# Kernel tuning notes

Measured on AMD Instinct MI355X. Metric: run time of the kernel, lower is better.

The kernel has to match this reference:

```python
import jax, jax.numpy as jnp
import numpy as np

B, N, C, NH = 32, 1024, 768, 12
KS = 3
KK = KS * KS
HD = C // NH
SCALE = HD ** -0.5
PMD = 2 * C   # patch_mix_dims = int(2 * dim)
CMD = 2 * C   # channel_mix_dims = int(2 * dim)


def _ln(x, g, b, eps):
    m = jnp.mean(x, axis=-1, keepdims=True)
    v = jnp.var(x, axis=-1, keepdims=True)
    return (x - m) * jax.lax.rsqrt(v + eps) * g + b


def setup_inputs() -> dict:
    key = jax.random.key(0)
    ks = jax.random.split(key, 12)
    w = lambda k, shape: jax.random.normal(k, shape, jnp.float32) * 0.02
    return dict(
        x=jax.random.normal(ks[0], (B, N, C), jnp.float32),
        H=32, W=32,
        kernel=w(ks[1], (KK, C)),                 # nn.Parameter, std 0.02
        ln_g=jnp.ones((C,), jnp.float32), ln_b=jnp.zeros((C,), jnp.float32),
        kv_w=w(ks[2], (C, 2 * C)),                # kv Linear, no bias (qkv_bias=False)
        proj_w=w(ks[3], (C, C)), proj_b=jnp.zeros((C,), jnp.float32),
        projq_w=w(ks[4], (C, C)),                 # proj_q, no bias
        n1_g=jnp.ones((C,), jnp.float32), n1_b=jnp.zeros((C,), jnp.float32),
        n2_g=jnp.ones((C,), jnp.float32), n2_b=jnp.zeros((C,), jnp.float32),
        pm1_w=w(ks[5], (KK, PMD)), pm1_b=jnp.zeros((PMD,), jnp.float32),
        pm2_w=w(ks[6], (PMD, KK)), pm2_b=jnp.zeros((KK,), jnp.float32),
        cm1_w=w(ks[7], (C, CMD)), cm1_b=jnp.zeros((CMD,), jnp.float32),
        cm2_w=w(ks[8], (CMD, C)), cm2_b=jnp.zeros((C,), jnp.float32),
    )


def reference(x, H, W, kernel, ln_g, ln_b, kv_w, proj_w, proj_b, projq_w,
              n1_g, n1_b, n2_g, n2_b, pm1_w, pm1_b, pm2_w, pm2_b,
              cm1_w, cm1_b, cm2_w, cm2_b):
    Bv, Nv, Cv = x.shape
    # w: expand learned 3x3 token kernel to batch -> [B, 9, C]
    w0 = jnp.broadcast_to(kernel, (Bv, KK, Cv))
    # queries from LN(kernel): [B, nh, 9, hd]
    wm = _ln(w0, ln_g, ln_b, 1e-6).reshape(Bv, KK, NH, HD).transpose(0, 2, 1, 3)
    # keys/values from x: [B, nh, N, hd]
    kv = (x @ kv_w).reshape(Bv, Nv, 2, NH, HD)
    k = kv[:, :, 0].transpose(0, 2, 1, 3)
    v = kv[:, :, 1].transpose(0, 2, 1, 3)
    attn = jax.nn.softmax(jnp.einsum('bhqd,bhkd->bhqk', wm, k) * SCALE, axis=-1)
    ca = jnp.einsum('bhqk,bhkd->bhqd', attn, v).transpose(0, 2, 1, 3).reshape(Bv, KK, Cv)
    ca = ca @ proj_w + proj_b
    w1 = w0 + ca                                  # [B, 9, C]
    # MLPMixer layer (drop_path = 0 -> identity)
    t = _ln(w1, n1_g, n1_b, 1e-5).transpose(0, 2, 1)              # [B, C, 9]
    t = jax.nn.gelu(t @ pm1_w + pm1_b, approximate=False) @ pm2_w + pm2_b
    w1 = w1 + t.transpose(0, 2, 1)
    t = _ln(w1, n2_g, n2_b, 1e-5)
    w1 = w1 + (jax.nn.gelu(t @ cm1_w + cm1_b, approximate=False) @ cm2_w + cm2_b)
    # dynamic per-(batch,channel) 3x3 depthwise conv
    filt = w1.transpose(0, 2, 1).reshape(Bv * Cv, 1, KS, KS)       # [B*C, 1, 3, 3]
    xq = (x @ projq_w).transpose(0, 2, 1).reshape(1, Bv * Cv, H, W)
    y = jax.lax.conv_general_dilated(
        xq, filt, window_strides=(1, 1), padding=((1, 1), (1, 1)),
        feature_group_count=Bv * Cv,
        dimension_numbers=('NCHW', 'OIHW', 'NCHW'))
    return y.reshape(Bv, Cv, H * W).transpose(0, 2, 1)             # [B, N, C]
```

## Files before the change

### kernel.cpp

```cpp
#include <hip/hip_runtime.h>
#include <hip/hip_bf16.h>
#include <cstdint>
#include <cstddef>

typedef __attribute__((ext_vector_type(8))) short bf16x8;
typedef __attribute__((ext_vector_type(4))) float f32x4;

#define BB 32
#define NN 1024
#define CC 768
#define NHH 12
#define HDD 64
#define KKK 9
#define MM (BB * NN)
#define KN2 1664
#define PMDD 1536
#define CMDD 1536
#define BK 64

#define XBF_BLOCKS 12288
#define WT_BLOCKS 1152
#define WT2_BLOCKS 2880
#define SW_BLOCKS 128

__device__ __forceinline__ float bfbits2f(short s) {
  union { uint32_t u; float f; } cv;
  cv.u = ((uint32_t)(uint16_t)s) << 16;
  return cv.f;
}
__device__ __forceinline__ short f2bf(float f) {
  union { float f; uint32_t u; } cv;
  cv.f = f;
  uint32_t u = cv.u;
  uint32_t r = (u + 0x7fffu + ((u >> 16) & 1u)) >> 16;
  return (short)r;
}
__device__ __forceinline__ float gelu_f(float x) {
  return 0.5f * x * (1.0f + erff(x * 0.7071067811865476f));
}

typedef const __attribute__((address_space(1))) uint32_t* gp1_t;
typedef __attribute__((address_space(3))) uint32_t* lp3_t;
__device__ __forceinline__ void gload16(const short* g, const short* l) {
  __builtin_amdgcn_global_load_lds((gp1_t)(uintptr_t)(const void*)g,
                                   (lp3_t)(uint32_t)(uintptr_t)(const void*)l,
                                   16, 0, 0);
}

__global__ __launch_bounds__(256) void prep_kernel(
    const float* __restrict__ x, short* __restrict__ xb,
    const float* __restrict__ kv_w, const float* __restrict__ projq_w,
    short* __restrict__ Wt,
    const float* __restrict__ proj_w, const float* __restrict__ cm1_w,
    const float* __restrict__ cm2_w,
    short* __restrict__ WpT, short* __restrict__ Wc1T, short* __restrict__ Wc2T,
    const float* __restrict__ kern, const float* __restrict__ ln_g,
    const float* __restrict__ ln_b)
{
  __shared__ float smem[1056];
  const int bx = blockIdx.x;
  const int tid = threadIdx.x;
  if (bx < XBF_BLOCKS) {
    const int i = (bx * 256 + tid) * 8;
    f32x4 a = *(const f32x4*)&x[i];
    f32x4 b = *(const f32x4*)&x[i + 4];
    bf16x8 o;
#pragma unroll
    for (int e = 0; e < 4; e++) { o[e] = f2bf(a[e]); o[e + 4] = f2bf(b[e]); }
    *(bf16x8*)&xb[i] = o;
    return;
  }
  if (bx < XBF_BLOCKS + WT_BLOCKS) {
    int b2 = bx - XBF_BLOCKS;
    int j0 = (b2 % 48) * 32;
    int c0 = (b2 / 48) * 32;
    const float* src; int ldj, jj;
    if (j0 < 768) { src = kv_w; ldj = 1536; jj = 768 + j0; }
    else          { src = projq_w; ldj = 768; jj = j0 - 768; }
    const int tx = tid & 31, ty = tid >> 5;
#pragma unroll
    for (int r = 0; r < 4; r++) {
      int cl = ty + r * 8;
      smem[cl * 33 + tx] = src[(size_t)(c0 + cl) * ldj + jj + tx];
    }
    __syncthreads();
#pragma unroll
    for (int r = 0; r < 4; r++) {
      int jl = ty + r * 8;
      Wt[(size_t)(j0 + jl) * CC + c0 + tx] = f2bf(smem[tx * 33 + jl]);
    }
    return;
  }
  if (bx < XBF_BLOCKS + WT_BLOCKS + WT2_BLOCKS) {
    int b2 = bx - XBF_BLOCKS - WT_BLOCKS;
    const float* src; short* dst; int ldj, ldc, j0, c0;
    if (b2 < 576)        { src = proj_w; dst = WpT;  ldj = 768;  ldc = 768;
                           j0 = (b2 % 24) * 32; c0 = (b2 / 24) * 32; }
    else if (b2 < 1728)  { b2 -= 576; src = cm1_w; dst = Wc1T; ldj = 1536; ldc = 768;
                           j0 = (b2 % 48) * 32; c0 = (b2 / 48) * 32; }
    else                 { b2 -= 1728; src = cm2_w; dst = Wc2T; ldj = 768; ldc = 1536;
                           j0 = (b2 % 24) * 32; c0 = (b2 / 24) * 32; }
    const int tx = tid & 31, ty = tid >> 5;
#pragma unroll
    for (int r = 0; r < 4; r++) {
      int cl = ty + r * 8;
      smem[cl * 33 + tx] = src[(size_t)(c0 + cl) * ldj + j0 + tx];
    }
    __syncthreads();
#pragma unroll
    for (int r = 0; r < 4; r++) {
      int jl = ty + r * 8;
      dst[(size_t)(j0 + jl) * ldc + c0 + tx] = f2bf(smem[tx * 33 + jl]);
    }
    return;
  }
  {
    const int s = bx - (XBF_BLOCKS + WT_BLOCKS + WT2_BLOCKS);
    if (s >= 108) {
      const size_t r = (size_t)(1536 + s) * CC;
      Wt[r + tid] = 0; Wt[r + tid + 256] = 0; Wt[r + tid + 512] = 0;
      return;
    }
    const int h = s / 9, q = s % 9;
    float* red = smem;
    const size_t base = (size_t)q * CC;
    float x0 = kern[base + tid];
    float x1 = kern[base + tid + 256];
    float x2 = kern[base + tid + 512];
    red[tid] = x0 + x1 + x2;
    __syncthreads();
    for (int st = 128; st > 0; st >>= 1) { if (tid < st) red[tid] += red[tid + st]; __syncthreads(); }
    float mean = red[0] * (1.0f / 768.0f);
    __syncthreads();
    float d0 = x0 - mean, d1 = x1 - mean, d2 = x2 - mean;
    red[tid] = d0 * d0 + d1 * d1 + d2 * d2;
    __syncthreads();
    for (int st = 128; st > 0; st >>= 1) { if (tid < st) red[tid] += red[tid + st]; __syncthreads(); }
    float rstd = rsqrtf(red[0] * (1.0f / 768.0f) + 1e-6f);
    __syncthreads();
    smem[tid]       = d0 * rstd * ln_g[tid]       + ln_b[tid];
    smem[tid + 256] = d1 * rstd * ln_g[tid + 256] + ln_b[tid + 256];
    smem[tid + 512] = d2 * rstd * ln_g[tid + 512] + ln_b[tid + 512];
    __syncthreads();
#pragma unroll
    for (int k = 0; k < 3; k++) {
      const int cc = tid + k * 256;
      const float* kw = &kv_w[(size_t)cc * 1536 + h * HDD];
      float acc = 0.f;
#pragma unroll
      for (int dd = 0; dd < HDD; dd++) acc += smem[h * HDD + dd] * kw[dd];
      Wt[(size_t)(1536 + s) * CC + cc] = f2bf(acc * 0.125f);
    }
  }
}

__global__ __launch_bounds__(256) void gemm_bt_kernel(
    const short* __restrict__ A,
    const short* __restrict__ Bt,
    short* __restrict__ C)
{
  __shared__ short As[128 * BK];
  __shared__ short Bs[128 * BK];
  const int tid = threadIdx.x;
  const int wave = tid >> 6, lane = tid & 63;
  const int lid = blockIdx.x;
  const int wid = (lid & 7) * 416 + (lid >> 3);
  const int bn = (wid % 13) * 128;
  const int bm = (wid / 13) * 128;
  const int wmo = (wave >> 1) * 64;
  const int wno = (wave & 1) * 64;
  const int lrow = lane & 15;
  const int kgrp = lane >> 4;
  const int sr = tid >> 3;
  const int ss = tid & 7;
  const int slotG = ss ^ (sr & 7);
  const short* gA = A + (size_t)(bm + sr) * CC + slotG * 8;
  const short* gB = Bt + (size_t)(bn + sr) * CC + slotG * 8;
  const short* lA = &As[sr * BK + ss * 8];
  const short* lB = &Bs[sr * BK + ss * 8];
  const int rs0 = kgrp ^ (lrow & 7);
  const int rs1 = (4 + kgrp) ^ (lrow & 7);
  f32x4 acc[4][4];
#pragma unroll
  for (int i = 0; i < 4; i++)
#pragma unroll
    for (int j = 0; j < 4; j++) acc[i][j] = (f32x4){0.f, 0.f, 0.f, 0.f};
  for (int k0 = 0; k0 < CC; k0 += BK) {
    __syncthreads();
#pragma unroll
    for (int i = 0; i < 4; i++) {
      gload16(gA + (size_t)(i * 32) * CC + k0, lA + i * 32 * BK);
      gload16(gB + (size_t)(i * 32) * CC + k0, lB + i * 32 * BK);
    }
    __syncthreads();
#pragma unroll
    for (int kh = 0; kh < 2; kh++) {
      const int rs = kh ? rs1 : rs0;
      bf16x8 af[4], bfr[4];
#pragma unroll
      for (int i = 0; i < 4; i++)
        af[i] = *(const bf16x8*)&As[(wmo + i * 16 + lrow) * BK + rs * 8];
#pragma unroll
      for (int j = 0; j < 4; j++)
        bfr[j] = *(const bf16x8*)&Bs[(wno + j * 16 + lrow) * BK + rs * 8];
#pragma unroll
      for (int i = 0; i < 4; i++)
#pragma unroll
        for (int j = 0; j < 4; j++)
          acc[i][j] = __builtin_amdgcn_mfma_f32_16x16x32_bf16(af[i], bfr[j], acc[i][j], 0, 0, 0);
    }
  }
#pragma unroll
  for (int i = 0; i < 4; i++)
#pragma unroll
    for (int j = 0; j < 4; j++)
#pragma unroll
      for (int r = 0; r < 4; r++) {
        const int row = bm + wmo + i * 16 + kgrp * 4 + r;
        const int col = bn + wno + j * 16 + lrow;
        C[(size_t)row * KN2 + col] = f2bf(acc[i][j][r]);
      }
}

template <int EP>
__global__ __launch_bounds__(256) void mfma96_kernel(
    const short* __restrict__ A,
    const short* __restrict__ Bt,
    int K, int ldn,
    const float* __restrict__ bias,
    const float* __restrict__ kern,
    float* __restrict__ Cf,
    short* __restrict__ Cb)
{
  __shared__ short As[96 * BK];
  __shared__ short Bs[128 * BK];
  const int tid = threadIdx.x;
  const int wave = tid >> 6, lane = tid & 63;
  const int bm = blockIdx.x * 96;
  const int bn = blockIdx.y * 128;
  const int wmo = (wave >> 1) * 48;
  const int wno = (wave & 1) * 64;
  const int lrow = lane & 15;
  const int kgrp = lane >> 4;
  const int sr = tid >> 3;
  const int ss = tid & 7;
  const int rs0 = kgrp ^ (lrow & 7);
  const int rs1 = (4 + kgrp) ^ (lrow & 7);
  f32x4 acc[3][4];
#pragma unroll
  for (int i = 0; i < 3; i++)
#pragma unroll
    for (int j = 0; j < 4; j++) acc[i][j] = (f32x4){0.f, 0.f, 0.f, 0.f};
  for (int k0 = 0; k0 < K; k0 += BK) {
    __syncthreads();
#pragma unroll
    for (int i = 0; i < 3; i++) {
      const int r = i * 32 + sr;
      const int sg = ss ^ (r & 7);
      gload16(A + (size_t)(bm + r) * K + k0 + sg * 8, &As[r * BK + ss * 8]);
    }
#pragma unroll
    for (int i = 0; i < 4; i++) {
      const int r = i * 32 + sr;
      const int sg = ss ^ (r & 7);
      gload16(Bt + (size_t)(bn + r) * K + k0 + sg * 8, &Bs[r * BK + ss * 8]);
    }
    __syncthreads();
#pragma unroll
    for (int kh = 0; kh < 2; kh++) {
      const int rs = kh ? rs1 : rs0;
      bf16x8 af[3], bfr[4];
#pragma unroll
      for (int m = 0; m < 3; m++)
        af[m] = *(const bf16x8*)&As[(wmo + m * 16 + lrow) * BK + rs * 8];
#pragma unroll
      for (int n = 0; n < 4; n++)
        bfr[n] = *(const bf16x8*)&Bs[(wno + n * 16 + lrow) * BK + rs * 8];
#pragma unroll
      for (int m = 0; m < 3; m++)
#pragma unroll
        for (int n = 0; n < 4; n++)
          acc[m][n] = __builtin_amdgcn_mfma_f32_16x16x32_bf16(af[m], bfr[n], acc[m][n], 0, 0, 0);
    }
  }
#pragma unroll
  for (int m = 0; m < 3; m++)
#pragma unroll
    for (int n = 0; n < 4; n++)
#pragma unroll
      for (int r = 0; r < 4; r++) {
        const int row = bm + wmo + m * 16 + kgrp * 4 + r;
        const int col = bn + wno + n * 16 + lrow;
        float v = acc[m][n][r] + bias[col];
        if (EP == 0) Cf[(size_t)row * ldn + col] = v + kern[(row % KKK) * ldn + col];
        if (EP == 1) Cb[(size_t)row * ldn + col] = f2bf(gelu_f(v));
        if (EP == 2) Cf[(size_t)row * ldn + col] += v;
      }
}

__global__ __launch_bounds__(256) void row_ln_bf_kernel(
    const float* __restrict__ in, short* __restrict__ out,
    const float* __restrict__ g, const float* __restrict__ bb, float eps)
{
  const int row = blockIdx.x;
  const int tid = threadIdx.x;
  __shared__ float red[256];
  const size_t base = (size_t)row * CC;
  float x0 = in[base + tid];
  float x1 = in[base + tid + 256];
  float x2 = in[base + tid + 512];
  red[tid] = x0 + x1 + x2;
  __syncthreads();
  for (int st = 128; st > 0; st >>= 1) { if (tid < st) red[tid] += red[tid + st]; __syncthreads(); }
  float mean = red[0] * (1.0f / 768.0f);
  __syncthreads();
  float d0 = x0 - mean, d1 = x1 - mean, d2 = x2 - mean;
  red[tid] = d0 * d0 + d1 * d1 + d2 * d2;
  __syncthreads();
  for (int st = 128; st > 0; st >>= 1) { if (tid < st) red[tid] += red[tid + st]; __syncthreads(); }
  float rstd = rsqrtf(red[0] * (1.0f / 768.0f) + eps);
  out[base + tid]       = f2bf(d0 * rstd * g[tid]       + bb[tid]);
  out[base + tid + 256] = f2bf(d1 * rstd * g[tid + 256] + bb[tid + 256]);
  out[base + tid + 512] = f2bf(d2 * rstd * g[tid + 512] + bb[tid + 512]);
}

__global__ __launch_bounds__(256) void attn_kernel(
    const short* __restrict__ big,
    short* __restrict__ ca)
{
  const int b = blockIdx.x;
  const int h = blockIdx.y;
  const int tid = threadIdx.x;
  const int wave = tid >> 6, lane = tid & 63;
  __shared__ float sc[KKK][NN];
  __shared__ float part[4][KKK][HDD];
#pragma unroll
  for (int nn = 0; nn < 4; nn++) {
    const int n = tid + nn * 256;
    const short* sp = &big[(size_t)(b * NN + n) * KN2 + 1536 + h * 9];
#pragma unroll
    for (int q = 0; q < KKK; q++) sc[q][n] = bfbits2f(sp[q]);
  }
  __syncthreads();
  for (int q = wave; q < KKK; q += 4) {
    float m = -1e30f;
#pragma unroll
    for (int i = 0; i < 16; i++) m = fmaxf(m, sc[q][lane + i * 64]);
#pragma unroll
    for (int off = 32; off > 0; off >>= 1) m = fmaxf(m, __shfl_xor(m, off));
    float s = 0.f;
#pragma unroll
    for (int i = 0; i < 16; i++) {
      float e = expf(sc[q][lane + i * 64] - m);
      sc[q][lane + i * 64] = e;
      s += e;
    }
#pragma unroll
    for (int off = 32; off > 0; off >>= 1) s += __shfl_xor(s, off);
    float inv = 1.0f / s;
#pragma unroll
    for (int i = 0; i < 16; i++) sc[q][lane + i * 64] *= inv;
  }
  __syncthreads();
  const int d = tid & 63, prt = tid >> 6;
  float po[KKK];
#pragma unroll
  for (int q = 0; q < KKK; q++) po[q] = 0.f;
  const short* vbase = &big[(size_t)(b * NN) * KN2 + h * HDD + d];
  for (int n0 = prt * 256; n0 < prt * 256 + 256; n0 += 4) {
    f32x4 p[KKK];
#pragma unroll
    for (int q = 0; q < KKK; q++) p[q] = *(const f32x4*)&sc[q][n0];
#pragma unroll
    for (int j = 0; j < 4; j++) {
      float vf = bfbits2f(vbase[(size_t)(n0 + j) * KN2]);
#pragma unroll
      for (int q = 0; q < KKK; q++) po[q] += p[q][j] * vf;
    }
  }
#pragma unroll
  for (int q = 0; q < KKK; q++) part[prt][q][d] = po[q];
  __syncthreads();
  for (int i = tid; i < KKK * HDD; i += 256) {
    int q = i >> 6, dd = i & 63;
    ca[(size_t)(b * KKK + q) * CC + h * HDD + dd] =
        f2bf(part[0][q][dd] + part[1][q][dd] + part[2][q][dd] + part[3][q][dd]);
  }
}

__global__ __launch_bounds__(256) void token_mix_kernel(
    const short* __restrict__ ln1,
    const float* __restrict__ pm1_w,
    const float* __restrict__ pm1_b,
    const float* __restrict__ pm2_w,
    float* __restrict__ part)
{
  const int tid = threadIdx.x;
  const int c = blockIdx.x * 256 + tid;
  const int b = blockIdx.y;
  const int jc = blockIdx.z;
  float u[KKK], o[KKK];
#pragma unroll
  for (int q = 0; q < KKK; q++) {
    u[q] = bfbits2f(ln1[(size_t)(b * KKK + q) * CC + c]);
    o[q] = 0.f;
  }
  const int j0 = jc * (PMDD / 8);
  for (int j = j0; j < j0 + PMDD / 8; j++) {
    float hs = pm1_b[j];
#pragma unroll
    for (int q = 0; q < KKK; q++) hs += u[q] * pm1_w[q * PMDD + j];
    float gv = gelu_f(hs);
    const float* p2 = &pm2_w[(size_t)j * KKK];
#pragma unroll
    for (int q = 0; q < KKK; q++) o[q] += gv * p2[q];
  }
  float* pp = &part[(size_t)((jc * BB + b) * KKK) * CC + c];
#pragma unroll
  for (int q = 0; q < KKK; q++) pp[(size_t)q * CC] = o[q];
}

__global__ __launch_bounds__(256) void token_reduce_ln_kernel(
    const float* __restrict__ part,
    const float* __restrict__ pm2_b,
    const float* __restrict__ g, const float* __restrict__ bb,
    float* __restrict__ w1,
    short* __restrict__ lnb)
{
  const int row = blockIdx.x;
  const int q = row % KKK;
  const int tid = threadIdx.x;
  __shared__ float red[256];
  const size_t base = (size_t)row * CC;
  float v[3];
#pragma unroll
  for (int j = 0; j < 3; j++) {
    const int c = tid + j * 256;
    float s = 0.f;
#pragma unroll
    for (int gg = 0; gg < 8; gg++)
      s += part[(size_t)gg * BB * KKK * CC + base + c];
    v[j] = w1[base + c] + s + pm2_b[q];
    w1[base + c] = v[j];
  }
  red[tid] = v[0] + v[1] + v[2];
  __syncthreads();
  for (int st = 128; st > 0; st >>= 1) { if (tid < st) red[tid] += red[tid + st]; __syncthreads(); }
  float mean = red[0] * (1.0f / 768.0f);
  __syncthreads();
  float d0 = v[0] - mean, d1 = v[1] - mean, d2 = v[2] - mean;
  red[tid] = d0 * d0 + d1 * d1 + d2 * d2;
  __syncthreads();
  for (int st = 128; st > 0; st >>= 1) { if (tid < st) red[tid] += red[tid + st]; __syncthreads(); }
  float rstd = rsqrtf(red[0] * (1.0f / 768.0f) + 1e-5f);
  lnb[base + tid]       = f2bf(d0 * rstd * g[tid]       + bb[tid]);
  lnb[base + tid + 256] = f2bf(d1 * rstd * g[tid + 256] + bb[tid + 256]);
  lnb[base + tid + 512] = f2bf(d2 * rstd * g[tid + 512] + bb[tid + 512]);
}

__global__ __launch_bounds__(256) void conv_lds_kernel(
    const short* __restrict__ big,
    const float* __restrict__ w1,
    float* __restrict__ out)
{
  __shared__ short rows[3][32][132];
  const int c0 = blockIdx.x * 128;
  const int b = blockIdx.y;
  const int y0 = blockIdx.z * 8;
  const int tid = threadIdx.x;
  const int xl = tid >> 3, cg = tid & 7;
  const int cl = tid & 127, xh = tid >> 7;
  float f[KKK];
#pragma unroll
  for (int q = 0; q < KKK; q++) f[q] = w1[(size_t)(b * KKK + q) * CC + c0 + cl];

#define LOAD_ROW(yy, slot)                                                     \
  {                                                                            \
    short* dst = &rows[slot][xl][cg * 16];                                     \
    if ((yy) >= 0 && (yy) < 32) {                                              \
      const short* src =                                                       \
          &big[(size_t)(b * NN + (yy) * 32 + xl) * KN2 + CC + c0 + cg * 16];   \
      *(bf16x8*)dst = *(const bf16x8*)src;                                     \
      *(bf16x8*)(dst + 8) = *(const bf16x8*)(src + 8);                         \
    } else {                                                                   \
      bf16x8 z = {0, 0, 0, 0, 0, 0, 0, 0};                                     \
      *(bf16x8*)dst = z;                                                       \
      *(bf16x8*)(dst + 8) = z;                                                 \
    }                                                                          \
  }

  int sPrev = 0, sCur = 1, sNext = 2;
  LOAD_ROW(y0 - 1, 0);
  LOAD_ROW(y0, 1);
  for (int y = y0; y < y0 + 8; ++y) {
    LOAD_ROW(y + 1, sNext);
    __syncthreads();
    const int xb = xh * 16;
    float v0[3], v1[3];
#pragma unroll
    for (int ky = 0; ky < 3; ky++) {
      const int s = (ky == 0) ? sPrev : (ky == 1 ? sCur : sNext);
      v1[ky] = bfbits2f(rows[s][xb][cl]);
      v0[ky] = (xb == 0) ? 0.f : bfbits2f(rows[s][xb - 1][cl]);
    }
    float* op = &out[(size_t)(b * NN + y * 32 + xb) * CC + c0 + cl];
#pragma unroll
    for (int i = 0; i < 16; i++) {
      const int x = xb + i;
      float v2[3];
#pragma unroll
      for (int ky = 0; ky < 3; ky++) {
        const int s = (ky == 0) ? sPrev : (ky == 1 ? sCur : sNext);
        v2[ky] = (x + 1 < 32) ? bfbits2f(rows[s][x + 1][cl]) : 0.f;
      }
      float acc = 0.f;
#pragma unroll
      for (int ky = 0; ky < 3; ky++)
        acc += f[ky * 3] * v0[ky] + f[ky * 3 + 1] * v1[ky] + f[ky * 3 + 2] * v2[ky];
      op[(size_t)i * CC] = acc;
#pragma unroll
      for (int ky = 0; ky < 3; ky++) { v0[ky] = v1[ky]; v1[ky] = v2[ky]; }
    }
    __syncthreads();
    const int t = sPrev; sPrev = sCur; sCur = sNext; sNext = t;
  }
#undef LOAD_ROW
}

extern "C" void kernel_launch(void* const* d_in, const int* in_sizes, int n_in,
                              void* d_out, int out_size, void* d_ws, size_t ws_size,
                              hipStream_t stream) {
  (void)in_sizes; (void)n_in; (void)out_size; (void)ws_size;
  const float* x       = (const float*)d_in[0];
  const float* kern    = (const float*)d_in[3];
  const float* ln_g    = (const float*)d_in[4];
  const float* ln_b    = (const float*)d_in[5];
  const float* kv_w    = (const float*)d_in[6];
  const float* proj_w  = (const float*)d_in[7];
  const float* proj_b  = (const float*)d_in[8];
  const float* projq_w = (const float*)d_in[9];
  const float* n1_g    = (const float*)d_in[10];
  const float* n1_b    = (const float*)d_in[11];
  const float* n2_g    = (const float*)d_in[12];
  const float* n2_b    = (const float*)d_in[13];
  const float* pm1_w   = (const float*)d_in[14];
  const float* pm1_b   = (const float*)d_in[15];
  const float* pm2_w   = (const float*)d_in[16];
  const float* pm2_b   = (const float*)d_in[17];
  const float* cm1_w   = (const float*)d_in[18];
  const float* cm1_b   = (const float*)d_in[19];
  const float* cm2_w   = (const float*)d_in[20];
  const float* cm2_b   = (const float*)d_in[21];
  float* out = (float*)d_out;

  uint8_t* ws = (uint8_t*)d_ws;
  short* Wt   = (short*)(ws);
  short* h1   = (short*)(ws);
  short* big  = (short*)(ws + 3538944);
  short* cab  = (short*)(ws + 154561536);
  float* w1   = (float*)(ws + 155446272);
  short* ln1b = (short*)(ws + 156331008);
  short* ln2b = (short*)(ws + 156773376);

  short* xb    = (short*)d_out;
  float* tpart = (float*)d_out;
  short* WpT   = (short*)((uint8_t*)d_out + 62914560);
  short* Wc1T  = (short*)((uint8_t*)d_out + 64094208);
  short* Wc2T  = (short*)((uint8_t*)d_out + 66453504);

  prep_kernel<<<dim3(XBF_BLOCKS + WT_BLOCKS + WT2_BLOCKS + SW_BLOCKS), 256, 0, stream>>>(
      x, xb, kv_w, projq_w, Wt, proj_w, cm1_w, cm2_w, WpT, Wc1T, Wc2T,
      kern, ln_g, ln_b);
  gemm_bt_kernel<<<dim3((MM / 128) * (KN2 / 128)), 256, 0, stream>>>(xb, Wt, big);
  attn_kernel<<<dim3(BB, NHH), 256, 0, stream>>>(big, cab);
  mfma96_kernel<0><<<dim3(3, 6), 256, 0, stream>>>(cab, WpT, CC, CC,
                                                   proj_b, kern, w1, nullptr);
  row_ln_bf_kernel<<<dim3(BB * KKK), 256, 0, stream>>>(w1, ln1b, n1_g, n1_b, 1e-5f);
  token_mix_kernel<<<dim3(3, 32, 8), 256, 0, stream>>>(ln1b, pm1_w, pm1_b, pm2_w, tpart);
  token_reduce_ln_kernel<<<dim3(BB * KKK), 256, 0, stream>>>(tpart, pm2_b,
                                                             n2_g, n2_b, w1, ln2b);
  mfma96_kernel<1><<<dim3(3, 12), 256, 0, stream>>>(ln2b, Wc1T, CC, CMDD,
                                                    cm1_b, nullptr, nullptr, h1);
  mfma96_kernel<2><<<dim3(3, 6), 256, 0, stream>>>(h1, Wc2T, CMDD, CC,
                                                   cm2_b, nullptr, w1, nullptr);
  conv_lds_kernel<<<dim3(6, 32, 4), 256, 0, stream>>>(big, w1, out);
}
```

Before: 372.4 us.

## Double-buffer LDS tiles in bf16 GEMM kernels to overlap loads with MFMA

Both the main KV/projection GEMM and the 96-row MFMA GEMM now use two LDS buffers. The next K-tile's global-to-LDS loads are issued before computing on the current tile, with explicit vmcnt waits and raw s_barriers replacing the two __syncthreads per iteration. The main GEMM also raises wave priority around its MFMA block. This is meant to hide global load latency behind matrix math, at the cost of doubling LDS use, which may reduce occupancy, and of relying on hand-counted vmcnt values being correct.

```diff
diff --git a/kernel.cpp b/kernel.cpp
--- a/kernel.cpp
+++ b/kernel.cpp
@@ -159,8 +159,8 @@
     const short* __restrict__ Bt,
     short* __restrict__ C)
 {
-  __shared__ short As[128 * BK];
-  __shared__ short Bs[128 * BK];
+  __shared__ short As[2][128 * BK];
+  __shared__ short Bs[2][128 * BK];
   const int tid = threadIdx.x;
   const int wave = tid >> 6, lane = tid & 63;
   const int lid = blockIdx.x;
@@ -176,8 +176,6 @@
   const int slotG = ss ^ (sr & 7);
   const short* gA = A + (size_t)(bm + sr) * CC + slotG * 8;
   const short* gB = Bt + (size_t)(bn + sr) * CC + slotG * 8;
-  const short* lA = &As[sr * BK + ss * 8];
-  const short* lB = &Bs[sr * BK + ss * 8];
   const int rs0 = kgrp ^ (lrow & 7);
   const int rs1 = (4 + kgrp) ^ (lrow & 7);
   f32x4 acc[4][4];
@@ -185,31 +183,49 @@
   for (int i = 0; i < 4; i++)
 #pragma unroll
     for (int j = 0; j < 4; j++) acc[i][j] = (f32x4){0.f, 0.f, 0.f, 0.f};
-  for (int k0 = 0; k0 < CC; k0 += BK) {
-    __syncthreads();
-#pragma unroll
-    for (int i = 0; i < 4; i++) {
-      gload16(gA + (size_t)(i * 32) * CC + k0, lA + i * 32 * BK);
-      gload16(gB + (size_t)(i * 32) * CC + k0, lB + i * 32 * BK);
-    }
-    __syncthreads();
+
+#define STAGE(bb, k0)                                                          \
+  {                                                                            \
+    _Pragma("unroll")                                                          \
+    for (int i = 0; i < 4; i++) {                                              \
+      gload16(gA + (size_t)(i * 32) * CC + (k0),                               \
+              &As[bb][(i * 32 + sr) * BK + ss * 8]);                           \
+      gload16(gB + (size_t)(i * 32) * CC + (k0),                               \
+              &Bs[bb][(i * 32 + sr) * BK + ss * 8]);                           \
+    }                                                                          \
+  }
+
+  STAGE(0, 0);
+  for (int t = 0; t < 12; ++t) {
+    const int cur = t & 1;
+    if (t < 11) STAGE(cur ^ 1, (t + 1) * BK);
+    __builtin_amdgcn_sched_barrier(0);
+    if (t < 11) asm volatile("s_waitcnt vmcnt(8)" ::: "memory");
+    else        asm volatile("s_waitcnt vmcnt(0)" ::: "memory");
+    __builtin_amdgcn_s_barrier();
+    __builtin_amdgcn_sched_barrier(0);
 #pragma unroll
     for (int kh = 0; kh < 2; kh++) {
       const int rs = kh ? rs1 : rs0;
       bf16x8 af[4], bfr[4];
 #pragma unroll
       for (int i = 0; i < 4; i++)
-        af[i] = *(const bf16x8*)&As[(wmo + i * 16 + lrow) * BK + rs * 8];
+        af[i] = *(const bf16x8*)&As[cur][(wmo + i * 16 + lrow) * BK + rs * 8];
 #pragma unroll
       for (int j = 0; j < 4; j++)
-        bfr[j] = *(const bf16x8*)&Bs[(wno + j * 16 + lrow) * BK + rs * 8];
+        bfr[j] = *(const bf16x8*)&Bs[cur][(wno + j * 16 + lrow) * BK + rs * 8];
+      __builtin_amdgcn_s_setprio(1);
 #pragma unroll
       for (int i = 0; i < 4; i++)
 #pragma unroll
         for (int j = 0; j < 4; j++)
           acc[i][j] = __builtin_amdgcn_mfma_f32_16x16x32_bf16(af[i], bfr[j], acc[i][j], 0, 0, 0);
-    }
-  }
+      __builtin_amdgcn_s_setprio(0);
+    }
+    __builtin_amdgcn_sched_barrier(0);
+    __builtin_amdgcn_s_barrier();
+  }
+#undef STAGE
 #pragma unroll
   for (int i = 0; i < 4; i++)
 #pragma unroll
@@ -232,8 +248,8 @@
     float* __restrict__ Cf,
     short* __restrict__ Cb)
 {
-  __shared__ short As[96 * BK];
-  __shared__ short Bs[128 * BK];
+  __shared__ short As[2][96 * BK];
+  __shared__ short Bs[2][128 * BK];
   const int tid = threadIdx.x;
   const int wave = tid >> 6, lane = tid & 63;
   const int bm = blockIdx.x * 96;
@@ -251,38 +267,55 @@
   for (int i = 0; i < 3; i++)
 #pragma unroll
     for (int j = 0; j < 4; j++) acc[i][j] = (f32x4){0.f, 0.f, 0.f, 0.f};
-  for (int k0 = 0; k0 < K; k0 += BK) {
-    __syncthreads();
-#pragma unroll
-    for (int i = 0; i < 3; i++) {
-      const int r = i * 32 + sr;
-      const int sg = ss ^ (r & 7);
-      gload16(A + (size_t)(bm + r) * K + k0 + sg * 8, &As[r * BK + ss * 8]);
-    }
-#pragma unroll
-    for (int i = 0; i < 4; i++) {
-      const int r = i * 32 + sr;
-      const int sg = ss ^ (r & 7);
-      gload16(Bt + (size_t)(bn + r) * K + k0 + sg * 8, &Bs[r * BK + ss * 8]);
-    }
-    __syncthreads();
+
+#define STAGEM(bb, k0)                                                         \
+  {                                                                            \
+    _Pragma("unroll")                                                          \
+    for (int i = 0; i < 3; i++) {                                              \
+      const int r = i * 32 + sr;                                               \
+      const int sg = ss ^ (r & 7);                                             \
+      gload16(A + (size_t)(bm + r) * K + (k0) + sg * 8,                        \
+              &As[bb][r * BK + ss * 8]);                                       \
+    }                                                                          \
+    _Pragma("unroll")                                                          \
+    for (int i = 0; i < 4; i++) {                                              \
+      const int r = i * 32 + sr;                                               \
+      const int sg = ss ^ (r & 7);                                             \
+      gload16(Bt + (size_t)(bn + r) * K + (k0) + sg * 8,                       \
+              &Bs[bb][r * BK + ss * 8]);                                       \
+    }                                                                          \
+  }
+
+  const int nt = K / BK;
+  STAGEM(0, 0);
+  for (int t = 0; t < nt; ++t) {
+    const int cur = t & 1;
+    if (t < nt - 1) STAGEM(cur ^ 1, (t + 1) * BK);
+    __builtin_amdgcn_sched_barrier(0);
+    if (t < nt - 1) asm volatile("s_waitcnt vmcnt(7)" ::: "memory");
+    else            asm volatile("s_waitcnt vmcnt(0)" ::: "memory");
+    __builtin_amdgcn_s_barrier();
+    __builtin_amdgcn_sched_barrier(0);
 #pragma unroll
     for (int kh = 0; kh < 2; kh++) {
       const int rs = kh ? rs1 : rs0;
       bf16x8 af[3], bfr[4];
 #pragma unroll
       for (int m = 0; m < 3; m++)
-        af[m] = *(const bf16x8*)&As[(wmo + m * 16 + lrow) * BK + rs * 8];
+        af[m] = *(const bf16x8*)&As[cur][(wmo + m * 16 + lrow) * BK + rs * 8];
 #pragma unroll
       for (int n = 0; n < 4; n++)
-        bfr[n] = *(const bf16x8*)&Bs[(wno + n * 16 + lrow) * BK + rs * 8];
+        bfr[n] = *(const bf16x8*)&Bs[cur][(wno + n * 16 + lrow) * BK + rs * 8];
 #pragma unroll
       for (int m = 0; m < 3; m++)
 #pragma unroll
         for (int n = 0; n < 4; n++)
           acc[m][n] = __builtin_amdgcn_mfma_f32_16x16x32_bf16(af[m], bfr[n], acc[m][n], 0, 0, 0);
     }
-  }
+    __builtin_amdgcn_sched_barrier(0);
+    __builtin_amdgcn_s_barrier();
+  }
+#undef STAGEM
 #pragma unroll
   for (int m = 0; m < 3; m++)
 #pragma unroll
```

After: 350.4 us. -5.9%, faster.
